# Performance work log

Measured on AMD Instinct MI355X. Metric: run time of the kernel, lower is better.

The kernel has to match this reference:

```python
import jax, jax.numpy as jnp
import numpy as np

EMB = 1024
HID = 1024
VOCAB = 50257


def _lstm_cell(x, h, c, Wih, Whh, bih, bhh):
    # PyTorch gate order: i, f, g, o
    gates = x @ Wih.T + bih + h @ Whh.T + bhh  # [1, 4H]
    i, f, g, o = jnp.split(gates, 4, axis=-1)
    c_new = jax.nn.sigmoid(f) * c + jax.nn.sigmoid(i) * jnp.tanh(g)
    h_new = jax.nn.sigmoid(o) * jnp.tanh(c_new)
    return h_new, c_new


def setup_inputs() -> dict:
    key = jax.random.key(0)
    ks = jax.random.split(key, 16)
    s = 0.02
    return {
        "word_input": jax.random.randint(ks[0], (1,), 0, VOCAB),
        "h0": jax.random.normal(ks[1], (2, 1, HID), jnp.float32),
        "c0": jax.random.normal(ks[2], (2, 1, HID), jnp.float32),
        "emb": jax.random.normal(ks[3], (VOCAB, EMB), jnp.float32) * s,
        "W_ih0": jax.random.normal(ks[4], (4 * HID, EMB), jnp.float32) * s,
        "W_hh0": jax.random.normal(ks[5], (4 * HID, HID), jnp.float32) * s,
        "b_ih0": jax.random.normal(ks[6], (4 * HID,), jnp.float32) * s,
        "b_hh0": jax.random.normal(ks[7], (4 * HID,), jnp.float32) * s,
        "W_ih1": jax.random.normal(ks[8], (4 * HID, HID), jnp.float32) * s,
        "W_hh1": jax.random.normal(ks[9], (4 * HID, HID), jnp.float32) * s,
        "b_ih1": jax.random.normal(ks[10], (4 * HID,), jnp.float32) * s,
        "b_hh1": jax.random.normal(ks[11], (4 * HID,), jnp.float32) * s,
        "W_out": jax.random.normal(ks[12], (VOCAB, HID), jnp.float32) * s,
        "b_out": jax.random.normal(ks[13], (VOCAB,), jnp.float32) * s,
    }


def reference(word_input, h0, c0, emb, W_ih0, W_hh0, b_ih0, b_hh0,
              W_ih1, W_hh1, b_ih1, b_hh1, W_out, b_out):
    # embedding lookup + ReLU, batch=1 seq=1
    x = jax.nn.relu(emb[word_input])                 # [1, EMB]
    # 2-layer LSTM single step (dropout disabled / eval mode)
    h1, c1 = _lstm_cell(x, h0[0], c0[0], W_ih0, W_hh0, b_ih0, b_hh0)
    h2, c2 = _lstm_cell(h1, h0[1], c0[1], W_ih1, W_hh1, b_ih1, b_hh1)
    logits = h2 @ W_out.T + b_out                    # [1, VOCAB]
    log_probas = jax.nn.log_softmax(logits, axis=1)
    h_out = jnp.stack([h1, h2])                      # [2, 1, HID]
    c_out = jnp.stack([c1, c2])
    return log_probas, (h_out, c_out)
```

## Files before the change

kernel.cpp:

```cpp
#include <hip/hip_runtime.h>
#include <math.h>

#define EMB 1024
#define HID 1024
#define VOCAB 50257
#define HOUT_OFF VOCAB
#define COUT_OFF (VOCAB + 2*HID)
#define ROWS_PER_BLOCK 16
#define NB_LOGITS ((VOCAB + ROWS_PER_BLOCK - 1) / ROWS_PER_BLOCK)

__device__ __forceinline__ float wave_reduce(float v) {
#pragma unroll
    for (int o = 32; o > 0; o >>= 1) v += __shfl_down(v, o);
    return v;
}

__device__ __forceinline__ float sigmoidf_(float x) { return 1.0f / (1.0f + expf(-x)); }

__global__ __launch_bounds__(256) void lstm_gemv(
    const float* __restrict__ Wih, const float* __restrict__ Whh,
    const float* __restrict__ bih, const float* __restrict__ bhh,
    const float* __restrict__ emb, const int* __restrict__ word,
    const float* __restrict__ x_in,
    const float* __restrict__ h_prev, const float* __restrict__ c_prev,
    float* __restrict__ h_ws, float* __restrict__ out, int layer)
{
    const int r    = blockIdx.x;
    const int wave = threadIdx.x >> 6;
    const int lane = threadIdx.x & 63;
    const int row  = wave * HID + r;

    float4 xv[4], hv[4];
    if (x_in != nullptr) {
#pragma unroll
        for (int j = 0; j < 4; ++j) xv[j] = ((const float4*)x_in)[j*64 + lane];
    } else {
        const float4* e = (const float4*)(emb + (size_t)word[0] * EMB);
#pragma unroll
        for (int j = 0; j < 4; ++j) {
            float4 v = e[j*64 + lane];
            v.x = fmaxf(v.x, 0.f); v.y = fmaxf(v.y, 0.f);
            v.z = fmaxf(v.z, 0.f); v.w = fmaxf(v.w, 0.f);
            xv[j] = v;
        }
    }
#pragma unroll
    for (int j = 0; j < 4; ++j) hv[j] = ((const float4*)h_prev)[j*64 + lane];

    const float4* wih = (const float4*)(Wih + (size_t)row * EMB);
    const float4* whh = (const float4*)(Whh + (size_t)row * HID);
    float acc = 0.f;
#pragma unroll
    for (int j = 0; j < 4; ++j) {
        float4 a = wih[j*64 + lane];
        acc += a.x*xv[j].x + a.y*xv[j].y + a.z*xv[j].z + a.w*xv[j].w;
        float4 b = whh[j*64 + lane];
        acc += b.x*hv[j].x + b.y*hv[j].y + b.z*hv[j].z + b.w*hv[j].w;
    }
    acc = wave_reduce(acc);

    __shared__ float gates[4];
    if (lane == 0) gates[wave] = acc + bih[row] + bhh[row];
    __syncthreads();

    if (threadIdx.x == 0) {
        float ig = sigmoidf_(gates[0]);
        float fg = sigmoidf_(gates[1]);
        float gg = tanhf(gates[2]);
        float og = sigmoidf_(gates[3]);
        float c  = fg * c_prev[r] + ig * gg;
        float h  = og * tanhf(c);
        h_ws[r] = h;
        out[HOUT_OFF + layer * HID + r] = h;
        out[COUT_OFF + layer * HID + r] = c;
    }
}

__global__ __launch_bounds__(256) void logits_gemv(
    const float* __restrict__ W, const float* __restrict__ b,
    const float* __restrict__ x, float* __restrict__ out,
    float* __restrict__ partials)
{
    const int wave = threadIdx.x >> 6;
    const int lane = threadIdx.x & 63;

    float4 xv[4];
#pragma unroll
    for (int j = 0; j < 4; ++j) xv[j] = ((const float4*)x)[j*64 + lane];

    float m = -INFINITY, s = 0.f;
    const int base = blockIdx.x * ROWS_PER_BLOCK + wave * 4;
#pragma unroll
    for (int k = 0; k < 4; ++k) {
        int row = base + k;
        if (row >= VOCAB) break;
        const float4* wr = (const float4*)(W + (size_t)row * HID);
        float acc = 0.f;
#pragma unroll
        for (int j = 0; j < 4; ++j) {
            float4 a = wr[j*64 + lane];
            acc += a.x*xv[j].x + a.y*xv[j].y + a.z*xv[j].z + a.w*xv[j].w;
        }
        acc = wave_reduce(acc);
        if (lane == 0) {
            float logit = acc + b[row];
            out[row] = logit;
            float nm = fmaxf(m, logit);
            s = s * expf(m - nm) + expf(logit - nm);
            m = nm;
        }
    }

    __shared__ float ms[4], ss[4];
    if (lane == 0) { ms[wave] = m; ss[wave] = s; }
    __syncthreads();
    if (threadIdx.x == 0) {
        float M = ms[0], S = ss[0];
#pragma unroll
        for (int w = 1; w < 4; ++w) {
            float nm = fmaxf(M, ms[w]);
            S = S * expf(M - nm) + ss[w] * expf(ms[w] - nm);
            M = nm;
        }
        partials[2 * blockIdx.x]     = M;
        partials[2 * blockIdx.x + 1] = S;
    }
}

__global__ __launch_bounds__(256) void softmax_combine(
    const float* __restrict__ partials, int nb, float* __restrict__ s_out)
{
    float M = -INFINITY, S = 0.f;
    for (int p = threadIdx.x; p < nb; p += 256) {
        float m = partials[2*p], s = partials[2*p + 1];
        float nm = fmaxf(M, m);
        S = S * expf(M - nm) + s * expf(m - nm);
        M = nm;
    }
    __shared__ float ms[256], ss[256];
    ms[threadIdx.x] = M; ss[threadIdx.x] = S;
    __syncthreads();
    for (int o = 128; o > 0; o >>= 1) {
        if (threadIdx.x < (unsigned)o) {
            float m2 = ms[threadIdx.x + o], s2 = ss[threadIdx.x + o];
            float m1 = ms[threadIdx.x];
            float nm = fmaxf(m1, m2);
            ss[threadIdx.x] = ss[threadIdx.x] * expf(m1 - nm) + s2 * expf(m2 - nm);
            ms[threadIdx.x] = nm;
        }
        __syncthreads();
    }
    if (threadIdx.x == 0) s_out[0] = ms[0] + logf(ss[0]);
}

__global__ __launch_bounds__(256) void logsoftmax_sub(
    float* __restrict__ out, const float* __restrict__ s_ptr, int n)
{
    int i = blockIdx.x * 256 + threadIdx.x;
    if (i < n) out[i] -= s_ptr[0];
}

extern "C" void kernel_launch(void* const* d_in, const int* in_sizes, int n_in,
                              void* d_out, int out_size, void* d_ws, size_t ws_size,
                              hipStream_t stream)
{
    const int*   word = (const int*)  d_in[0];
    const float* h0   = (const float*)d_in[1];
    const float* c0   = (const float*)d_in[2];
    const float* emb  = (const float*)d_in[3];
    const float* Wih0 = (const float*)d_in[4];
    const float* Whh0 = (const float*)d_in[5];
    const float* bih0 = (const float*)d_in[6];
    const float* bhh0 = (const float*)d_in[7];
    const float* Wih1 = (const float*)d_in[8];
    const float* Whh1 = (const float*)d_in[9];
    const float* bih1 = (const float*)d_in[10];
    const float* bhh1 = (const float*)d_in[11];
    const float* Wout = (const float*)d_in[12];
    const float* bout = (const float*)d_in[13];

    float* out = (float*)d_out;
    float* ws  = (float*)d_ws;
    float* h1       = ws;
    float* h2       = ws + HID;
    float* partials = ws + 2 * HID;
    float* s_ptr    = ws + 2 * HID + 2 * NB_LOGITS;

    lstm_gemv<<<HID, 256, 0, stream>>>(Wih0, Whh0, bih0, bhh0, emb, word,
                                       nullptr, h0, c0, h1, out, 0);
    lstm_gemv<<<HID, 256, 0, stream>>>(Wih1, Whh1, bih1, bhh1, emb, word,
                                       h1, h0 + HID, c0 + HID, h2, out, 1);
    logits_gemv<<<NB_LOGITS, 256, 0, stream>>>(Wout, bout, h2, out, partials);
    softmax_combine<<<1, 256, 0, stream>>>(partials, NB_LOGITS, s_ptr);
    logsoftmax_sub<<<(VOCAB + 255) / 256, 256, 0, stream>>>(out, s_ptr, VOCAB);
}
```

Before: 436.0 us.

## Use 16-lane row groups in logits GEMV and fuse softmax combine into subtract

The logits GEMV now assigns 16 threads per vocabulary row, so each wave handles four rows at once with four independent accumulators and a short 16-lane shuffle reduce, instead of one wave per row looping serially. The separate single-block softmax_combine kernel is removed: every block of the subtract kernel now redundantly reduces the ~3141 partials itself and then subtracts the log-normalizer. This saves one launch and a serialized tiny kernel, at the cost of repeated partial reductions across about 197 blocks and a different memory access pattern for the weight rows.

```diff
diff --git a/kernel.cpp b/kernel.cpp
--- a/kernel.cpp
+++ b/kernel.cpp
@@ -6,8 +6,8 @@
 #define VOCAB 50257
 #define HOUT_OFF VOCAB
 #define COUT_OFF (VOCAB + 2*HID)
-#define ROWS_PER_BLOCK 16
-#define NB_LOGITS ((VOCAB + ROWS_PER_BLOCK - 1) / ROWS_PER_BLOCK)
+#define RPB 16
+#define NB_LOGITS ((VOCAB + RPB - 1) / RPB)
 
 __device__ __forceinline__ float wave_reduce(float v) {
 #pragma unroll
@@ -81,54 +81,61 @@
     const float* __restrict__ x, float* __restrict__ out,
     float* __restrict__ partials)
 {
-    const int wave = threadIdx.x >> 6;
-    const int lane = threadIdx.x & 63;
+    const int tid = threadIdx.x;
+    const int l   = tid & 15;
+    const int row = blockIdx.x * RPB + (tid >> 4);
 
-    float4 xv[4];
-#pragma unroll
-    for (int j = 0; j < 4; ++j) xv[j] = ((const float4*)x)[j*64 + lane];
+    __shared__ float lg[RPB];
+    if (tid < RPB) lg[tid] = -INFINITY;
+    __syncthreads();
 
-    float m = -INFINITY, s = 0.f;
-    const int base = blockIdx.x * ROWS_PER_BLOCK + wave * 4;
-#pragma unroll
-    for (int k = 0; k < 4; ++k) {
-        int row = base + k;
-        if (row >= VOCAB) break;
-        const float4* wr = (const float4*)(W + (size_t)row * HID);
-        float acc = 0.f;
+    float a0 = 0.f, a1 = 0.f, a2 = 0.f, a3 = 0.f;
+    if (row < VOCAB) {
+        const float4* __restrict__ wr = (const float4*)(W + (size_t)row * HID);
+        const float4* __restrict__ xp = (const float4*)x;
 #pragma unroll
         for (int j = 0; j < 4; ++j) {
-            float4 a = wr[j*64 + lane];
-            acc += a.x*xv[j].x + a.y*xv[j].y + a.z*xv[j].z + a.w*xv[j].w;
-        }
-        acc = wave_reduce(acc);
-        if (lane == 0) {
-            float logit = acc + b[row];
-            out[row] = logit;
-            float nm = fmaxf(m, logit);
-            s = s * expf(m - nm) + expf(logit - nm);
-            m = nm;
+            float4 w0 = wr[l + 16*(4*j+0)], x0 = xp[l + 16*(4*j+0)];
+            float4 w1 = wr[l + 16*(4*j+1)], x1 = xp[l + 16*(4*j+1)];
+            float4 w2 = wr[l + 16*(4*j+2)], x2 = xp[l + 16*(4*j+2)];
+            float4 w3 = wr[l + 16*(4*j+3)], x3 = xp[l + 16*(4*j+3)];
+            a0 += w0.x*x0.x + w0.y*x0.y + w0.z*x0.z + w0.w*x0.w;
+            a1 += w1.x*x1.x + w1.y*x1.y + w1.z*x1.z + w1.w*x1.w;
+            a2 += w2.x*x2.x + w2.y*x2.y + w2.z*x2.z + w2.w*x2.w;
+            a3 += w3.x*x3.x + w3.y*x3.y + w3.z*x3.z + w3.w*x3.w;
         }
     }
+    float acc = (a0 + a1) + (a2 + a3);
+    acc += __shfl_xor(acc, 8);
+    acc += __shfl_xor(acc, 4);
+    acc += __shfl_xor(acc, 2);
+    acc += __shfl_xor(acc, 1);
 
-    __shared__ float ms[4], ss[4];
-    if (lane == 0) { ms[wave] = m; ss[wave] = s; }
+    if (l == 0 && row < VOCAB) {
+        float logit = acc + b[row];
+        out[row] = logit;
+        lg[tid >> 4] = logit;
+    }
     __syncthreads();
-    if (threadIdx.x == 0) {
-        float M = ms[0], S = ss[0];
+
+    if (tid == 0) {
+        float M = -INFINITY, S = 0.f;
 #pragma unroll
-        for (int w = 1; w < 4; ++w) {
-            float nm = fmaxf(M, ms[w]);
-            S = S * expf(M - nm) + ss[w] * expf(ms[w] - nm);
-            M = nm;
+        for (int i = 0; i < RPB; ++i) {
+            float v = lg[i];
+            if (v > -INFINITY) {
+                float nm = fmaxf(M, v);
+                S = S * expf(M - nm) + expf(v - nm);
+                M = nm;
+            }
         }
         partials[2 * blockIdx.x]     = M;
         partials[2 * blockIdx.x + 1] = S;
     }
 }
 
-__global__ __launch_bounds__(256) void softmax_combine(
-    const float* __restrict__ partials, int nb, float* __restrict__ s_out)
+__global__ __launch_bounds__(256) void logsoftmax_sub(
+    float* __restrict__ out, const float* __restrict__ partials, int nb, int n)
 {
     float M = -INFINITY, S = 0.f;
     for (int p = threadIdx.x; p < nb; p += 256) {
@@ -150,14 +157,9 @@
         }
         __syncthreads();
     }
-    if (threadIdx.x == 0) s_out[0] = ms[0] + logf(ss[0]);
-}
-
-__global__ __launch_bounds__(256) void logsoftmax_sub(
-    float* __restrict__ out, const float* __restrict__ s_ptr, int n)
-{
+    float Z = ms[0] + logf(ss[0]);
     int i = blockIdx.x * 256 + threadIdx.x;
-    if (i < n) out[i] -= s_ptr[0];
+    if (i < n) out[i] -= Z;
 }
 
 extern "C" void kernel_launch(void* const* d_in, const int* in_sizes, int n_in,
@@ -184,13 +186,12 @@
     float* h1       = ws;
     float* h2       = ws + HID;
     float* partials = ws + 2 * HID;
-    float* s_ptr    = ws + 2 * HID + 2 * NB_LOGITS;
 
     lstm_gemv<<<HID, 256, 0, stream>>>(Wih0, Whh0, bih0, bhh0, emb, word,
                                        nullptr, h0, c0, h1, out, 0);
     lstm_gemv<<<HID, 256, 0, stream>>>(Wih1, Whh1, bih1, bhh1, emb, word,
                                        h1, h0 + HID, c0 + HID, h2, out, 1);
     logits_gemv<<<NB_LOGITS, 256, 0, stream>>>(Wout, bout, h2, out, partials);
-    softmax_combine<<<1, 256, 0, stream>>>(partials, NB_LOGITS, s_ptr);
-    logsoftmax_sub<<<(VOCAB + 255) / 256, 256, 0, stream>>>(out, s_ptr, VOCAB);
+    logsoftmax_sub<<<(VOCAB + 255) / 256, 256, 0, stream>>>(out, partials,
+                                                            NB_LOGITS, VOCAB);
 }
```

Measured after the change: 438.3 us. Within noise of the previous version (+0.5%).
